# Kernel tuning notes

Measured on AMD Instinct MI355X. Metric: run time of the kernel, lower is better.

## Reference

```python
import jax, jax.numpy as jnp
import numpy as np

B, L, K, H, D = 2, 512, 128, 32, 1024
NUM_EDGES = 2048
SQRT_2PI = 2.5066282746310002
MIN_F32 = float(np.finfo(np.float32).min)
SCALING = K ** -0.5


def setup_inputs() -> dict:
    key = jax.random.key(0)
    ks = jax.random.split(key, 18)
    pos = jax.random.normal(ks[0], (B, L, 3), jnp.float32) * 10.0
    node_type_edge = jax.random.randint(ks[1], (B, L, L, 2), 0, NUM_EDGES)
    adj = jax.random.randint(ks[2], (B, L, L), 0, 2).astype(bool)
    # last 64 tokens of second sample are padding
    padding_mask = jnp.arange(L)[None, :] >= jnp.array([L, L - 64])[:, None]
    molecule_mask = jax.random.randint(ks[3], (B, L), 0, 2).astype(bool)
    clean_mask = jax.random.randint(ks[4], (B, L), 0, 2).astype(bool)
    # parameters
    pos_emb_w = jax.random.normal(ks[5], (K, 3), jnp.float32) * 0.1            # nn.Linear(3, K, bias=False)
    pos_feature_emb_w = jax.random.normal(ks[6], (D, K), jnp.float32) * (K ** -0.5)  # nn.Linear(K, D, bias=False)
    gbf_means = jax.random.uniform(ks[7], (K,), jnp.float32, minval=0.0, maxval=3.0)
    gbf_stds = jax.random.uniform(ks[8], (K,), jnp.float32, minval=0.1, maxval=3.0)
    gbf_mul = jax.random.normal(ks[9], (NUM_EDGES, 1), jnp.float32) * 0.1 + 1.0
    gbf_bias = jax.random.normal(ks[10], (NUM_EDGES, 1), jnp.float32) * 0.1
    proj_w1 = jax.random.normal(ks[11], (K, K), jnp.float32) * (K ** -0.5)     # NonLinear layer1
    proj_b1 = jnp.zeros((K,), jnp.float32)
    proj_w2 = jax.random.normal(ks[12], (H, K), jnp.float32) * (K ** -0.5)     # NonLinear layer2
    proj_b2 = jnp.zeros((H,), jnp.float32)
    pos_proj_w = jax.random.normal(ks[13], (D, K), jnp.float32) * (K ** -0.5)  # pos_embedding_proj
    pos_proj_b = jnp.zeros((D,), jnp.float32)
    return dict(pos=pos, node_type_edge=node_type_edge, adj=adj, padding_mask=padding_mask,
                molecule_mask=molecule_mask, clean_mask=clean_mask,
                pos_emb_w=pos_emb_w, pos_feature_emb_w=pos_feature_emb_w,
                gbf_means=gbf_means, gbf_stds=gbf_stds, gbf_mul=gbf_mul, gbf_bias=gbf_bias,
                proj_w1=proj_w1, proj_b1=proj_b1, proj_w2=proj_w2, proj_b2=proj_b2,
                pos_proj_w=pos_proj_w, pos_proj_b=pos_proj_b)


def reference(pos, node_type_edge, adj, padding_mask, molecule_mask, clean_mask,
              pos_emb_w, pos_feature_emb_w, gbf_means, gbf_stds, gbf_mul, gbf_bias,
              proj_w1, proj_b1, proj_w2, proj_b2, pos_proj_w, pos_proj_b):
    # pairwise distances [B,L,L] (eps-safe sqrt; grad at diagonal is 0)
    delta = pos[:, :, None, :] - pos[:, None, :, :]
    dist0 = jnp.sqrt(jnp.sum(delta * delta, axis=-1) + 1e-12)

    # adj forced True on non-molecule / clean rows
    adj = jnp.where(~molecule_mask[:, :, None], True, adj)
    adj = jnp.where(clean_mask[:, :, None], True, adj)

    # GaussianLayer: per-edge-type affine on dist, then K gaussian kernels -> [B,L,L,K]
    mul = gbf_mul[node_type_edge].sum(axis=-2)    # [B,L,L,1]
    bia = gbf_bias[node_type_edge].sum(axis=-2)   # [B,L,L,1]
    x = mul * dist0[..., None] + bia              # [B,L,L,1]
    std = jnp.abs(gbf_stds) + 1e-5                # [K]
    edge_feature = jnp.exp(-0.5 * jnp.square((x - gbf_means) / std)) / (SQRT_2PI * std)  # [B,L,L,K]

    # NonLinear projection to heads
    h = jax.nn.gelu(jnp.einsum('blmk,jk->blmj', edge_feature, proj_w1) + proj_b1, approximate=False)
    gab = jnp.einsum('blmj,nj->blmn', h, proj_w2) + proj_b2   # [B,L,L,H]

    expand_mask = padding_mask
    gab = jnp.where(expand_mask[:, None, :, None], -jnp.inf, gab)
    gab = jnp.where(~adj[..., None], -jnp.inf, gab)
    gab = jnp.where(padding_mask[:, :, None, None], 0.0, gab)
    graph_attn_bias = jnp.transpose(gab, (0, 3, 1, 2))        # [B,H,L,L]

    dist = graph_attn_bias.sum(axis=1)                        # [B,L,L]
    dist = jnp.where(expand_mask[:, None, :], MIN_F32, dist)
    dist = jnp.where(padding_mask[:, :, None], MIN_F32, dist)

    pos_emb = jnp.einsum('blc,kc->blk', pos, pos_emb_w)       # [B,L,K]
    pos_emb = jnp.where(expand_mask[..., None], 0.0, pos_emb)

    dist = jnp.where(~adj, MIN_F32, dist)
    dist = jax.nn.softmax(dist.astype(jnp.float32) * SCALING, axis=-1)

    pfe = jnp.einsum('blm,bmk->blk', dist, pos_emb)           # weighted aggregation
    pfe = jnp.einsum('blk,dk->bld', pfe, pos_feature_emb_w)   # Linear(K, D, bias=False)

    ef = jnp.where(expand_mask[:, None, :, None], 0.0, edge_feature).sum(axis=-2)  # [B,L,K]
    pfe = pfe + jnp.einsum('blk,dk->bld', ef, pos_proj_w) + pos_proj_b
    pfe = jnp.where(padding_mask[..., None], 0.0, pfe)
    return pfe, graph_attn_bias
```

## Files before the change

### kernel.cpp

```cpp
#include <hip/hip_runtime.h>
#include <hip/hip_bf16.h>

typedef __attribute__((ext_vector_type(8))) short short8;
typedef __attribute__((ext_vector_type(4))) float f32x4;

static const int BB = 2;
static const int LL = 512;
#define MIN_F32 (-3.4028234663852886e+38f)
#define NEG_BIG (-1.0e38f)
#define SCALING_F 0.08838834764831845f
#define SQ2PI 2.5066282746310002f

__device__ __forceinline__ float gelu_fast(float x) {
    float s  = x * 0.70710678118654752440f;
    float za = fabsf(s);
    float t  = __builtin_amdgcn_rcpf(fmaf(za, 0.3275911f, 1.0f));
    float p  = t * fmaf(t, fmaf(t, fmaf(t, fmaf(t, 1.061405429f, -1.453152027f),
                                        1.421413741f), -0.284496736f), 0.254829592f);
    float e  = __expf(-za * za);
    float q  = fmaf(-p, e, 1.0f);
    union { float f; unsigned u; } uq, us;
    uq.f = q; us.f = s;
    uq.u = (uq.u & 0x7FFFFFFFu) | (us.u & 0x80000000u);
    float hx = 0.5f * x;
    return fmaf(hx, uq.f, hx);
}
__device__ __forceinline__ unsigned pack_bf16x2(float lo, float hi) {
    __hip_bfloat162 h2 = __float22bfloat162_rn(float2{lo, hi});
    union { __hip_bfloat162 h; unsigned u; } v; v.h = h2;
    return v.u;
}
__device__ __forceinline__ unsigned short f2bf(float f) {
    union { float f; unsigned int u; } v; v.f = f;
    unsigned int u = v.u;
    return (unsigned short)((u + 0x7FFFu + ((u >> 16) & 1u)) >> 16);
}
__device__ __forceinline__ int swz(int row, int bytecol) {
    return row * 256 + (bytecol ^ ((row & 7) << 4));
}

__global__ __launch_bounds__(256) void prep_kernel(
    const float* __restrict__ wfe, const float* __restrict__ wp,
    float* __restrict__ wfet, float* __restrict__ wpt)
{
    int idx = blockIdx.x * 256 + threadIdx.x;
    int which = idx >> 17;
    int r = idx & 131071;
    int k = r >> 10;
    int d = r & 1023;
    if (which == 0) wfet[r] = wfe[d * 128 + k];
    else            wpt[r]  = wp[d * 128 + k];
}

__global__ __launch_bounds__(512, 4) void row_kernel(
    const float* __restrict__ pos,
    const int*   __restrict__ nte,
    const unsigned char* __restrict__ adj,
    const unsigned char* __restrict__ padm,
    const unsigned char* __restrict__ molm,
    const unsigned char* __restrict__ clnm,
    const float* __restrict__ gmean,
    const float* __restrict__ gstd,
    const float* __restrict__ gmul,
    const float* __restrict__ gbias,
    const float* __restrict__ w1,
    const float* __restrict__ b1,
    const float* __restrict__ w2,
    const float* __restrict__ b2,
    const float* __restrict__ pw,
    float* __restrict__ out_gab,
    float* __restrict__ pfe1,
    float* __restrict__ efsum)
{
    __shared__ __align__(16) char W1s[128 * 256];
    __shared__ __align__(16) char W2s[32 * 256];
    __shared__ __align__(16) char efs[64 * 256];
    __shared__ __align__(16) char hs [64 * 256];
    __shared__ float dist_row[512];
    __shared__ float xval[512];
    __shared__ unsigned char flgall[512];
    __shared__ float b1s[128];
    __shared__ float b2s[32];
    __shared__ float sred[16];
    __shared__ float dsump[128];

    const int t = threadIdx.x;
    const int row = blockIdx.x;
    const int b = row >> 9;
    const int i = row & 511;

    const int w  = t >> 6;
    const int l  = t & 63;
    const int lr = l & 15;
    const int lq = l >> 4;

    for (int idx = t; idx < 2048 + 512; idx += 512) {
        const float* src; char* dst; int r16, c16;
        if (idx < 2048) { r16 = idx >> 4;          c16 = idx & 15; src = w1 + r16 * 128 + c16 * 8; dst = W1s; }
        else            { r16 = (idx - 2048) >> 4; c16 = (idx - 2048) & 15; src = w2 + r16 * 128 + c16 * 8; dst = W2s; }
        float4 f0 = *(const float4*)(src);
        float4 f1 = *(const float4*)(src + 4);
        uint4 pk;
        pk.x = (unsigned)f2bf(f0.x) | ((unsigned)f2bf(f0.y) << 16);
        pk.y = (unsigned)f2bf(f0.z) | ((unsigned)f2bf(f0.w) << 16);
        pk.z = (unsigned)f2bf(f1.x) | ((unsigned)f2bf(f1.y) << 16);
        pk.w = (unsigned)f2bf(f1.z) | ((unsigned)f2bf(f1.w) << 16);
        *(uint4*)(dst + swz(r16, c16 * 16)) = pk;
    }
    if (t < 128) b1s[t] = b1[t];
    if (t < 32)  b2s[t] = b2[t];

    const bool pad_i = padm[row] != 0;
    const bool force_adj = (clnm[row] != 0) || (molm[row] == 0);
    const float pix = pos[row * 3 + 0], piy = pos[row * 3 + 1], piz = pos[row * 3 + 2];

    {
        int2 e2 = ((const int2*)nte)[row * 512 + t];
        float mul = gmul[e2.x] + gmul[e2.y];
        float bia = gbias[e2.x] + gbias[e2.y];
        float dx = pix - pos[(b * 512 + t) * 3 + 0];
        float dy = piy - pos[(b * 512 + t) * 3 + 1];
        float dz = piz - pos[(b * 512 + t) * 3 + 2];
        float dist = sqrtf(dx * dx + dy * dy + dz * dz + 1e-12f);
        xval[t] = mul * dist + bia;
        int padj = padm[b * 512 + t] ? 1 : 0;
        int adje = (force_adj || adj[row * 512 + t]) ? 2 : 0;
        flgall[t] = (unsigned char)(padj | adje);
    }

    const int k0 = (t & 15) * 8;
    const int js = t >> 4;
    float mean_q[8], istd_q[8], lnc_q[8], efacc[8];
    #pragma unroll
    for (int q = 0; q < 8; ++q) {
        float gsv = fabsf(gstd[k0 + q]) + 1e-5f;
        mean_q[q] = gmean[k0 + q];
        istd_q[q] = 1.0f / gsv;
        lnc_q[q]  = -logf(SQ2PI * gsv);
        efacc[q]  = 0.f;
    }

    __syncthreads();

    for (int tile = 0; tile < 8; ++tile) {
        const int j0 = tile * 64;
        if (tile > 0 && t < 64) {
            int fl = flgall[j0 - 64 + t];
            bool masked = pad_i || (fl & 1) || !(fl & 2);
            dist_row[j0 - 64 + t] = masked ? MIN_F32 : (dsump[t] + dsump[64 + t]);
        }
        #pragma unroll
        for (int jj = 0; jj < 2; ++jj) {
            int j = js + jj * 32;
            float x  = xval[j0 + j];
            float mk = (flgall[j0 + j] & 1) ? 0.0f : 1.0f;
            unsigned pk[4];
            #pragma unroll
            for (int q = 0; q < 4; ++q) {
                float a0 = (x - mean_q[2*q+0]) * istd_q[2*q+0];
                float a1 = (x - mean_q[2*q+1]) * istd_q[2*q+1];
                float e0 = __expf(fmaf(a0 * a0, -0.5f, lnc_q[2*q+0]));
                float e1 = __expf(fmaf(a1 * a1, -0.5f, lnc_q[2*q+1]));
                efacc[2*q+0] = fmaf(e0, mk, efacc[2*q+0]);
                efacc[2*q+1] = fmaf(e1, mk, efacc[2*q+1]);
                pk[q] = pack_bf16x2(e0, e1);
            }
            *(uint4*)(efs + swz(j, 2 * k0)) = make_uint4(pk[0], pk[1], pk[2], pk[3]);
        }
        __syncthreads();
        {
            const int jobase = (w & 3) * 32;
            const int jbase  = (w >> 2) * 32;
            f32x4 a00 = {0.f,0.f,0.f,0.f}, a01 = a00, a10 = a00, a11 = a00;
            #pragma unroll
            for (int ks = 0; ks < 4; ++ks) {
                int bcol = ks * 64 + lq * 16;
                short8 av0 = *(const short8*)(W1s + swz(jobase + lr, bcol));
                short8 av1 = *(const short8*)(W1s + swz(jobase + 16 + lr, bcol));
                short8 bv0 = *(const short8*)(efs + swz(jbase + lr, bcol));
                short8 bv1 = *(const short8*)(efs + swz(jbase + 16 + lr, bcol));
                a00 = __builtin_amdgcn_mfma_f32_16x16x32_bf16(av0, bv0, a00, 0, 0, 0);
                a01 = __builtin_amdgcn_mfma_f32_16x16x32_bf16(av0, bv1, a01, 0, 0, 0);
                a10 = __builtin_amdgcn_mfma_f32_16x16x32_bf16(av1, bv0, a10, 0, 0, 0);
                a11 = __builtin_amdgcn_mfma_f32_16x16x32_bf16(av1, bv1, a11, 0, 0, 0);
            }
            #pragma unroll
            for (int mi = 0; mi < 2; ++mi) {
                int jo0 = jobase + mi * 16 + lq * 4;
                float4 bb = *(const float4*)&b1s[jo0];
                #pragma unroll
                for (int ci = 0; ci < 2; ++ci) {
                    f32x4 acc = (mi == 0) ? (ci == 0 ? a00 : a01) : (ci == 0 ? a10 : a11);
                    int j = jbase + ci * 16 + lr;
                    float g0 = gelu_fast(acc[0] + bb.x);
                    float g1 = gelu_fast(acc[1] + bb.y);
                    float g2 = gelu_fast(acc[2] + bb.z);
                    float g3 = gelu_fast(acc[3] + bb.w);
                    uint2 pv = make_uint2(pack_bf16x2(g0, g1), pack_bf16x2(g2, g3));
                    *(uint2*)(hs + swz(j, 2 * jo0)) = pv;
                }
            }
        }
        __syncthreads();
        {
            const int mt = w >> 2;
            const int jt2 = w & 3;
            f32x4 acc = (f32x4){0.f, 0.f, 0.f, 0.f};
            #pragma unroll
            for (int ks = 0; ks < 4; ++ks) {
                int bcol = ks * 64 + lq * 16;
                short8 av = *(const short8*)(W2s + swz(mt * 16 + lr, bcol));
                short8 bv = *(const short8*)(hs + swz(jt2 * 16 + lr, bcol));
                acc = __builtin_amdgcn_mfma_f32_16x16x32_bf16(av, bv, acc, 0, 0, 0);
            }
            int jl = jt2 * 16 + lr;
            int jg = j0 + jl;
            int fl = flgall[jg];
            bool kill = (fl & 1) || !(fl & 2);
            float dpart = 0.f;
            size_t base = ((size_t)(b * 32 + mt * 16 + lq * 4) * 512 + i) * 512 + jg;
            #pragma unroll
            for (int r = 0; r < 4; ++r) {
                float raw = acc[r] + b2s[mt * 16 + lq * 4 + r];
                dpart += raw;
                float outv = pad_i ? 0.0f : (kill ? NEG_BIG : raw);
                out_gab[base + (size_t)r * 262144] = outv;
            }
            dpart += __shfl_xor(dpart, 16);
            dpart += __shfl_xor(dpart, 32);
            if (l < 16) dsump[mt * 64 + jl] = dpart;
        }
        __syncthreads();
    }

    float* rb = (float*)efs;
    if (t < 64) {
        int fl = flgall[448 + t];
        bool masked = pad_i || (fl & 1) || !(fl & 2);
        dist_row[448 + t] = masked ? MIN_F32 : (dsump[t] + dsump[64 + t]);
    }
    *(float4*)&rb[t * 8 + 0] = make_float4(efacc[0], efacc[1], efacc[2], efacc[3]);
    *(float4*)&rb[t * 8 + 4] = make_float4(efacc[4], efacc[5], efacc[6], efacc[7]);
    __syncthreads();
    if (t < 128) {
        float s = 0.f;
        #pragma unroll
        for (int sidx = 0; sidx < 32; ++sidx) s += rb[sidx * 128 + t];
        efsum[(size_t)row * 128 + t] = s;
    }

    float sv = dist_row[t] * SCALING_F;
    float v = sv;
    #pragma unroll
    for (int m = 32; m > 0; m >>= 1) v = fmaxf(v, __shfl_xor(v, m));
    if ((t & 63) == 0) sred[t >> 6] = v;
    __syncthreads();
    float mx = sred[0];
    #pragma unroll
    for (int w8 = 1; w8 < 8; ++w8) mx = fmaxf(mx, sred[w8]);
    float e = expf(sv - mx);
    v = e;
    #pragma unroll
    for (int m = 32; m > 0; m >>= 1) v += __shfl_xor(v, m);
    if ((t & 63) == 0) sred[8 + (t >> 6)] = v;
    __syncthreads();
    float sm = 0.f;
    #pragma unroll
    for (int w8 = 0; w8 < 8; ++w8) sm += sred[8 + w8];
    float p = e / sm;

    float px = pos[(b * 512 + t) * 3 + 0];
    float py = pos[(b * 512 + t) * 3 + 1];
    float pz = pos[(b * 512 + t) * 3 + 2];
    float vx = p * px, vy = p * py, vz = p * pz;
    #pragma unroll
    for (int m = 32; m > 0; m >>= 1) {
        vx += __shfl_xor(vx, m); vy += __shfl_xor(vy, m); vz += __shfl_xor(vz, m);
    }
    __syncthreads();
    if ((t & 63) == 0) {
        int w8 = t >> 6;
        rb[w8] = vx; rb[8 + w8] = vy; rb[16 + w8] = vz;
    }
    __syncthreads();
    if (t < 128) {
        float w0 = 0.f, w1v = 0.f, w2v = 0.f;
        #pragma unroll
        for (int w8 = 0; w8 < 8; ++w8) {
            w0 += rb[w8]; w1v += rb[8 + w8]; w2v += rb[16 + w8];
        }
        pfe1[(size_t)row * 128 + t] = pw[t * 3 + 0] * w0 + pw[t * 3 + 1] * w1v + pw[t * 3 + 2] * w2v;
    }
}

__global__ __launch_bounds__(256) void pfe_kernel(
    const float* __restrict__ pfe1,
    const float* __restrict__ efsum,
    const float* __restrict__ wfet,
    const float* __restrict__ wpt,
    const float* __restrict__ pb,
    const unsigned char* __restrict__ padm,
    float* __restrict__ out)
{
    __shared__ __align__(16) float As[2 * 32 * 132];
    __shared__ __align__(16) float Bs[2 * 16 * 128];
    const int t  = threadIdx.x;
    const int tx = t & 31;
    const int ty = t >> 5;
    const int r0 = (blockIdx.x >> 3) * 32;
    const int d0 = (blockIdx.x & 7) * 128;

    #pragma unroll
    for (int q = 0; q < 16; ++q) {
        int ii = t + q * 256;
        int r = ii >> 7, k = ii & 127;
        As[(0 * 32 + r) * 132 + k] = pfe1 [(size_t)(r0 + r) * 128 + k];
        As[(1 * 32 + r) * 132 + k] = efsum[(size_t)(r0 + r) * 128 + k];
    }

    f32x4 acc[4];
    #pragma unroll
    for (int rr = 0; rr < 4; ++rr) acc[rr] = (f32x4){0.f, 0.f, 0.f, 0.f};

    for (int kc = 0; kc < 8; ++kc) {
        __syncthreads();
        #pragma unroll
        for (int q = 0; q < 2; ++q) {
            int ii = t + q * 256;
            int kr = ii >> 5, dq = ii & 31;
            f32x4 v0 = ((const f32x4*)(wfet + (size_t)(kc * 16 + kr) * 1024 + d0))[dq];
            f32x4 v1 = ((const f32x4*)(wpt  + (size_t)(kc * 16 + kr) * 1024 + d0))[dq];
            *(f32x4*)&Bs[(0 * 16 + kr) * 128 + dq * 4] = v0;
            *(f32x4*)&Bs[(1 * 16 + kr) * 128 + dq * 4] = v1;
        }
        __syncthreads();
        #pragma unroll
        for (int k4 = 0; k4 < 4; ++k4) {
            int kb = kc * 16 + k4 * 4;
            f32x4 a0[4], a1[4];
            #pragma unroll
            for (int rr = 0; rr < 4; ++rr) {
                int r = ty * 4 + rr;
                a0[rr] = *(const f32x4*)&As[(0 * 32 + r) * 132 + kb];
                a1[rr] = *(const f32x4*)&As[(1 * 32 + r) * 132 + kb];
            }
            #pragma unroll
            for (int kq = 0; kq < 4; ++kq) {
                f32x4 b0 = *(const f32x4*)&Bs[(0 * 16 + k4 * 4 + kq) * 128 + tx * 4];
                f32x4 b1 = *(const f32x4*)&Bs[(1 * 16 + k4 * 4 + kq) * 128 + tx * 4];
                #pragma unroll
                for (int rr = 0; rr < 4; ++rr) {
                    acc[rr] += a0[rr][kq] * b0 + a1[rr][kq] * b1;
                }
            }
        }
    }

    f32x4 bv = *(const f32x4*)&pb[d0 + tx * 4];
    #pragma unroll
    for (int rr = 0; rr < 4; ++rr) {
        int row = r0 + ty * 4 + rr;
        f32x4 o = acc[rr] + bv;
        if (padm[row]) o = (f32x4){0.f, 0.f, 0.f, 0.f};
        *(f32x4*)&out[(size_t)row * 1024 + d0 + tx * 4] = o;
    }
}

extern "C" void kernel_launch(void* const* d_in, const int* in_sizes, int n_in,
                              void* d_out, int out_size, void* d_ws, size_t ws_size,
                              hipStream_t stream) {
    const float* pos  = (const float*)d_in[0];
    const int*   nte  = (const int*)d_in[1];
    const unsigned char* adj  = (const unsigned char*)d_in[2];
    const unsigned char* padm = (const unsigned char*)d_in[3];
    const unsigned char* molm = (const unsigned char*)d_in[4];
    const unsigned char* clnm = (const unsigned char*)d_in[5];
    const float* pw    = (const float*)d_in[6];
    const float* wfe   = (const float*)d_in[7];
    const float* gmean = (const float*)d_in[8];
    const float* gstd  = (const float*)d_in[9];
    const float* gmul  = (const float*)d_in[10];
    const float* gbias = (const float*)d_in[11];
    const float* w1    = (const float*)d_in[12];
    const float* b1    = (const float*)d_in[13];
    const float* w2    = (const float*)d_in[14];
    const float* b2    = (const float*)d_in[15];
    const float* wp    = (const float*)d_in[16];
    const float* pb    = (const float*)d_in[17];

    float* out      = (float*)d_out;
    float* out_pfe  = out;
    float* out_gab  = out + (size_t)BB * LL * 1024;

    float* ws    = (float*)d_ws;
    float* pfe1  = ws;
    float* efsum = ws + 131072;
    float* wfet  = ws + 262144;
    float* wpt   = ws + 393216;

    prep_kernel<<<1024, 256, 0, stream>>>(wfe, wp, wfet, wpt);
    row_kernel<<<BB * LL, 512, 0, stream>>>(pos, nte, adj, padm, molm, clnm,
                                            gmean, gstd, gmul, gbias,
                                            w1, b1, w2, b2, pw,
                                            out_gab, pfe1, efsum);
    pfe_kernel<<<256, 256, 0, stream>>>(pfe1, efsum, wfet, wpt, pb, padm, out_pfe);
}
```

Baseline: 115.8 us.

## Make each wave own a 16-column slice, removing block-wide barriers in edge MLP

The per-tile cooperative pipeline, which used shared efs/hs buffers and three __syncthreads per tile, is replaced by a per-wave scheme. Each wave computes Gaussian features for its own 16 columns, runs both MLP layers on them in a private 4KB LDS buffer, and writes dist_row directly. W2 now lives in register fragments rather than LDS. The Gaussian exponent is rewritten in base 2 and uses the hardware v_exp_f32 instruction. The cost is more W1 LDS reads per wave, since each wave now reads the full W1, and higher register pressure from holding the W2 fragments.

```diff
diff --git a/kernel.cpp b/kernel.cpp
--- a/kernel.cpp
+++ b/kernel.cpp
@@ -11,6 +11,9 @@
 #define SCALING_F 0.08838834764831845f
 #define SQ2PI 2.5066282746310002f
 
+__device__ __forceinline__ float exp2_hw(float x) {
+    float r; asm("v_exp_f32 %0, %1" : "=v"(r) : "v"(x)); return r;
+}
 __device__ __forceinline__ float gelu_fast(float x) {
     float s  = x * 0.70710678118654752440f;
     float za = fabsf(s);
@@ -73,16 +76,13 @@
     float* __restrict__ efsum)
 {
     __shared__ __align__(16) char W1s[128 * 256];
-    __shared__ __align__(16) char W2s[32 * 256];
-    __shared__ __align__(16) char efs[64 * 256];
-    __shared__ __align__(16) char hs [64 * 256];
+    __shared__ __align__(16) char wbuf[8][4096];
     __shared__ float dist_row[512];
     __shared__ float xval[512];
     __shared__ unsigned char flgall[512];
     __shared__ float b1s[128];
     __shared__ float b2s[32];
     __shared__ float sred[16];
-    __shared__ float dsump[128];
 
     const int t = threadIdx.x;
     const int row = blockIdx.x;
@@ -94,10 +94,9 @@
     const int lr = l & 15;
     const int lq = l >> 4;
 
-    for (int idx = t; idx < 2048 + 512; idx += 512) {
-        const float* src; char* dst; int r16, c16;
-        if (idx < 2048) { r16 = idx >> 4;          c16 = idx & 15; src = w1 + r16 * 128 + c16 * 8; dst = W1s; }
-        else            { r16 = (idx - 2048) >> 4; c16 = (idx - 2048) & 15; src = w2 + r16 * 128 + c16 * 8; dst = W2s; }
+    for (int idx = t; idx < 2048; idx += 512) {
+        int r16 = idx >> 4, c16 = idx & 15;
+        const float* src = w1 + r16 * 128 + c16 * 8;
         float4 f0 = *(const float4*)(src);
         float4 f1 = *(const float4*)(src + 4);
         uint4 pk;
@@ -105,7 +104,7 @@
         pk.y = (unsigned)f2bf(f0.z) | ((unsigned)f2bf(f0.w) << 16);
         pk.z = (unsigned)f2bf(f1.x) | ((unsigned)f2bf(f1.y) << 16);
         pk.w = (unsigned)f2bf(f1.z) | ((unsigned)f2bf(f1.w) << 16);
-        *(uint4*)(dst + swz(r16, c16 * 16)) = pk;
+        *(uint4*)(W1s + swz(r16, c16 * 16)) = pk;
     }
     if (t < 128) b1s[t] = b1[t];
     if (t < 32)  b2s[t] = b2[t];
@@ -128,117 +127,125 @@
         flgall[t] = (unsigned char)(padj | adje);
     }
 
-    const int k0 = (t & 15) * 8;
-    const int js = t >> 4;
+    short8 w2f0[4], w2f1[4];
+    #pragma unroll
+    for (int ks = 0; ks < 4; ++ks) {
+        const float* s0 = w2 + (0 * 16 + lr) * 128 + ks * 32 + lq * 8;
+        const float* s1 = w2 + (1 * 16 + lr) * 128 + ks * 32 + lq * 8;
+        float4 a0 = *(const float4*)s0, a1 = *(const float4*)(s0 + 4);
+        float4 c0 = *(const float4*)s1, c1 = *(const float4*)(s1 + 4);
+        union { uint4 u; short8 s; } cv;
+        cv.u = make_uint4(pack_bf16x2(a0.x, a0.y), pack_bf16x2(a0.z, a0.w),
+                          pack_bf16x2(a1.x, a1.y), pack_bf16x2(a1.z, a1.w));
+        w2f0[ks] = cv.s;
+        cv.u = make_uint4(pack_bf16x2(c0.x, c0.y), pack_bf16x2(c0.z, c0.w),
+                          pack_bf16x2(c1.x, c1.y), pack_bf16x2(c1.z, c1.w));
+        w2f1[ks] = cv.s;
+    }
+
+    const int k0 = lr * 8;
     float mean_q[8], istd_q[8], lnc_q[8], efacc[8];
     #pragma unroll
     for (int q = 0; q < 8; ++q) {
         float gsv = fabsf(gstd[k0 + q]) + 1e-5f;
         mean_q[q] = gmean[k0 + q];
-        istd_q[q] = 1.0f / gsv;
-        lnc_q[q]  = -logf(SQ2PI * gsv);
+        istd_q[q] = 0.84932180f / gsv;
+        lnc_q[q]  = -log2f(SQ2PI * gsv);
         efacc[q]  = 0.f;
     }
 
     __syncthreads();
 
-    for (int tile = 0; tile < 8; ++tile) {
-        const int j0 = tile * 64;
-        if (tile > 0 && t < 64) {
-            int fl = flgall[j0 - 64 + t];
-            bool masked = pad_i || (fl & 1) || !(fl & 2);
-            dist_row[j0 - 64 + t] = masked ? MIN_F32 : (dsump[t] + dsump[64 + t]);
-        }
-        #pragma unroll
-        for (int jj = 0; jj < 2; ++jj) {
-            int j = js + jj * 32;
-            float x  = xval[j0 + j];
-            float mk = (flgall[j0 + j] & 1) ? 0.0f : 1.0f;
+    char* myb = wbuf[w];
+    for (int rnd = 0; rnd < 4; ++rnd) {
+        const int jbase = rnd * 128 + w * 16;
+        #pragma unroll
+        for (int jj = 0; jj < 4; ++jj) {
+            int jloc = lq + jj * 4;
+            int j = jbase + jloc;
+            float x  = xval[j];
+            float mk = (flgall[j] & 1) ? 0.0f : 1.0f;
             unsigned pk[4];
             #pragma unroll
             for (int q = 0; q < 4; ++q) {
                 float a0 = (x - mean_q[2*q+0]) * istd_q[2*q+0];
                 float a1 = (x - mean_q[2*q+1]) * istd_q[2*q+1];
-                float e0 = __expf(fmaf(a0 * a0, -0.5f, lnc_q[2*q+0]));
-                float e1 = __expf(fmaf(a1 * a1, -0.5f, lnc_q[2*q+1]));
+                float e0 = exp2_hw(fmaf(a0, -a0, lnc_q[2*q+0]));
+                float e1 = exp2_hw(fmaf(a1, -a1, lnc_q[2*q+1]));
                 efacc[2*q+0] = fmaf(e0, mk, efacc[2*q+0]);
                 efacc[2*q+1] = fmaf(e1, mk, efacc[2*q+1]);
                 pk[q] = pack_bf16x2(e0, e1);
             }
-            *(uint4*)(efs + swz(j, 2 * k0)) = make_uint4(pk[0], pk[1], pk[2], pk[3]);
-        }
-        __syncthreads();
-        {
-            const int jobase = (w & 3) * 32;
-            const int jbase  = (w >> 2) * 32;
-            f32x4 a00 = {0.f,0.f,0.f,0.f}, a01 = a00, a10 = a00, a11 = a00;
+            *(uint4*)(myb + swz(jloc, 2 * k0)) = make_uint4(pk[0], pk[1], pk[2], pk[3]);
+        }
+        short8 eff[4];
+        #pragma unroll
+        for (int ks = 0; ks < 4; ++ks)
+            eff[ks] = *(const short8*)(myb + swz(lr, ks * 64 + lq * 16));
+        #pragma unroll
+        for (int half = 0; half < 2; ++half) {
+            f32x4 acc0 = {0.f,0.f,0.f,0.f}, acc1 = acc0, acc2 = acc0, acc3 = acc0;
+            const int cb = half * 4;
             #pragma unroll
             for (int ks = 0; ks < 4; ++ks) {
                 int bcol = ks * 64 + lq * 16;
-                short8 av0 = *(const short8*)(W1s + swz(jobase + lr, bcol));
-                short8 av1 = *(const short8*)(W1s + swz(jobase + 16 + lr, bcol));
-                short8 bv0 = *(const short8*)(efs + swz(jbase + lr, bcol));
-                short8 bv1 = *(const short8*)(efs + swz(jbase + 16 + lr, bcol));
-                a00 = __builtin_amdgcn_mfma_f32_16x16x32_bf16(av0, bv0, a00, 0, 0, 0);
-                a01 = __builtin_amdgcn_mfma_f32_16x16x32_bf16(av0, bv1, a01, 0, 0, 0);
-                a10 = __builtin_amdgcn_mfma_f32_16x16x32_bf16(av1, bv0, a10, 0, 0, 0);
-                a11 = __builtin_amdgcn_mfma_f32_16x16x32_bf16(av1, bv1, a11, 0, 0, 0);
-            }
-            #pragma unroll
-            for (int mi = 0; mi < 2; ++mi) {
-                int jo0 = jobase + mi * 16 + lq * 4;
+                short8 av0 = *(const short8*)(W1s + swz((cb+0)*16 + lr, bcol));
+                short8 av1 = *(const short8*)(W1s + swz((cb+1)*16 + lr, bcol));
+                short8 av2 = *(const short8*)(W1s + swz((cb+2)*16 + lr, bcol));
+                short8 av3 = *(const short8*)(W1s + swz((cb+3)*16 + lr, bcol));
+                acc0 = __builtin_amdgcn_mfma_f32_16x16x32_bf16(av0, eff[ks], acc0, 0, 0, 0);
+                acc1 = __builtin_amdgcn_mfma_f32_16x16x32_bf16(av1, eff[ks], acc1, 0, 0, 0);
+                acc2 = __builtin_amdgcn_mfma_f32_16x16x32_bf16(av2, eff[ks], acc2, 0, 0, 0);
+                acc3 = __builtin_amdgcn_mfma_f32_16x16x32_bf16(av3, eff[ks], acc3, 0, 0, 0);
+            }
+            #pragma unroll
+            for (int ci = 0; ci < 4; ++ci) {
+                f32x4 acc = (ci == 0) ? acc0 : (ci == 1) ? acc1 : (ci == 2) ? acc2 : acc3;
+                int jo0 = (cb + ci) * 16 + lq * 4;
                 float4 bb = *(const float4*)&b1s[jo0];
-                #pragma unroll
-                for (int ci = 0; ci < 2; ++ci) {
-                    f32x4 acc = (mi == 0) ? (ci == 0 ? a00 : a01) : (ci == 0 ? a10 : a11);
-                    int j = jbase + ci * 16 + lr;
-                    float g0 = gelu_fast(acc[0] + bb.x);
-                    float g1 = gelu_fast(acc[1] + bb.y);
-                    float g2 = gelu_fast(acc[2] + bb.z);
-                    float g3 = gelu_fast(acc[3] + bb.w);
-                    uint2 pv = make_uint2(pack_bf16x2(g0, g1), pack_bf16x2(g2, g3));
-                    *(uint2*)(hs + swz(j, 2 * jo0)) = pv;
-                }
-            }
-        }
-        __syncthreads();
-        {
-            const int mt = w >> 2;
-            const int jt2 = w & 3;
-            f32x4 acc = (f32x4){0.f, 0.f, 0.f, 0.f};
-            #pragma unroll
-            for (int ks = 0; ks < 4; ++ks) {
-                int bcol = ks * 64 + lq * 16;
-                short8 av = *(const short8*)(W2s + swz(mt * 16 + lr, bcol));
-                short8 bv = *(const short8*)(hs + swz(jt2 * 16 + lr, bcol));
-                acc = __builtin_amdgcn_mfma_f32_16x16x32_bf16(av, bv, acc, 0, 0, 0);
-            }
-            int jl = jt2 * 16 + lr;
-            int jg = j0 + jl;
-            int fl = flgall[jg];
-            bool kill = (fl & 1) || !(fl & 2);
-            float dpart = 0.f;
+                float g0 = gelu_fast(acc[0] + bb.x);
+                float g1 = gelu_fast(acc[1] + bb.y);
+                float g2 = gelu_fast(acc[2] + bb.z);
+                float g3 = gelu_fast(acc[3] + bb.w);
+                *(uint2*)(myb + swz(lr, 2 * jo0)) =
+                    make_uint2(pack_bf16x2(g0, g1), pack_bf16x2(g2, g3));
+            }
+        }
+        f32x4 acc20 = {0.f,0.f,0.f,0.f}, acc21 = acc20;
+        #pragma unroll
+        for (int ks = 0; ks < 4; ++ks) {
+            short8 hf = *(const short8*)(myb + swz(lr, ks * 64 + lq * 16));
+            acc20 = __builtin_amdgcn_mfma_f32_16x16x32_bf16(w2f0[ks], hf, acc20, 0, 0, 0);
+            acc21 = __builtin_amdgcn_mfma_f32_16x16x32_bf16(w2f1[ks], hf, acc21, 0, 0, 0);
+        }
+        int jg = jbase + lr;
+        int fl = flgall[jg];
+        bool kill = (fl & 1) || !(fl & 2);
+        float dpart = 0.f;
+        #pragma unroll
+        for (int mt = 0; mt < 2; ++mt) {
+            f32x4 acc = mt ? acc21 : acc20;
+            float4 bb = *(const float4*)&b2s[mt * 16 + lq * 4];
             size_t base = ((size_t)(b * 32 + mt * 16 + lq * 4) * 512 + i) * 512 + jg;
             #pragma unroll
             for (int r = 0; r < 4; ++r) {
-                float raw = acc[r] + b2s[mt * 16 + lq * 4 + r];
+                float raw = acc[r] + ((const float*)&bb)[r];
                 dpart += raw;
                 float outv = pad_i ? 0.0f : (kill ? NEG_BIG : raw);
                 out_gab[base + (size_t)r * 262144] = outv;
             }
-            dpart += __shfl_xor(dpart, 16);
-            dpart += __shfl_xor(dpart, 32);
-            if (l < 16) dsump[mt * 64 + jl] = dpart;
-        }
-        __syncthreads();
-    }
-
-    float* rb = (float*)efs;
-    if (t < 64) {
-        int fl = flgall[448 + t];
-        bool masked = pad_i || (fl & 1) || !(fl & 2);
-        dist_row[448 + t] = masked ? MIN_F32 : (dsump[t] + dsump[64 + t]);
-    }
+        }
+        dpart += __shfl_xor(dpart, 16);
+        dpart += __shfl_xor(dpart, 32);
+        if (l < 16) {
+            bool masked = pad_i || kill;
+            dist_row[jg] = masked ? MIN_F32 : dpart;
+        }
+    }
+
+    __syncthreads();
+
+    float* rb = (float*)wbuf;
     *(float4*)&rb[t * 8 + 0] = make_float4(efacc[0], efacc[1], efacc[2], efacc[3]);
     *(float4*)&rb[t * 8 + 4] = make_float4(efacc[4], efacc[5], efacc[6], efacc[7]);
     __syncthreads();
```

Result: slower. 169.3 us (+46.2%).
